# Performance work log

Hardware: AMD Instinct MI355X
Metric: run time of the kernel (lower is better)

The kernel has to match this reference:

```python
import math
import jax, jax.numpy as jnp
import numpy as np

H, DK = 16, 64            # n_heads, d_kv
NUM_BUCKETS, MAX_DIST = 32, 128


def _relative_position_buckets(S):
    # Bidirectional (encoder) T5 bucketization of relative positions.
    ctx = jnp.arange(S, dtype=jnp.int32)[:, None]      # query positions
    mem = jnp.arange(S, dtype=jnp.int32)[None, :]      # key positions
    rp = mem - ctx                                     # [S, S]
    nb = NUM_BUCKETS // 2
    rb = (rp > 0).astype(jnp.int32) * nb
    n = jnp.abs(rp)
    max_exact = nb // 2
    is_small = n < max_exact
    large = max_exact + (
        jnp.log(jnp.maximum(n, 1).astype(jnp.float32) / max_exact)
        / math.log(MAX_DIST / max_exact)
        * (nb - max_exact)
    ).astype(jnp.int32)
    large = jnp.minimum(large, nb - 1)
    return rb + jnp.where(is_small, n, large)          # [S, S] int32


def setup_inputs() -> dict:
    key = jax.random.key(0)
    ks = jax.random.split(key, 6)
    B, S, D = 4, 1024, 1024
    inner = H * DK
    std = 0.02
    return {
        "hidden_states": jax.random.normal(ks[0], (B, S, D), jnp.float32),
        "Wq": jax.random.normal(ks[1], (inner, D), jnp.float32) * std,
        "Wk": jax.random.normal(ks[2], (inner, D), jnp.float32) * std,
        "Wv": jax.random.normal(ks[3], (inner, D), jnp.float32) * std,
        "Wo": jax.random.normal(ks[4], (D, inner), jnp.float32) * std,
        "rel_bias": jax.random.normal(ks[5], (NUM_BUCKETS, H), jnp.float32) * std,
    }


def reference(hidden_states, Wq, Wk, Wv, Wo, rel_bias):
    B, S, D = hidden_states.shape

    def proj(W):  # bias-free linear + split heads -> [B, H, S, DK]
        return (hidden_states @ W.T).reshape(B, S, H, DK).transpose(0, 2, 1, 3)

    q, k, v = proj(Wq), proj(Wk), proj(Wv)
    # T5: NO 1/sqrt(d) scaling
    scores = jnp.einsum("bhqd,bhkd->bhqk", q, k)       # [B, H, S, S]
    bias = rel_bias[_relative_position_buckets(S)]     # [S, S, H]
    scores = scores + bias.transpose(2, 0, 1)[None]    # broadcast over batch
    attn = jax.nn.softmax(scores, axis=-1)
    ctx = jnp.einsum("bhqk,bhkd->bhqd", attn, v)       # [B, H, S, DK]
    ctx = ctx.transpose(0, 2, 1, 3).reshape(B, S, H * DK)
    return ctx @ Wo.T                                  # [B, S, D]
```

## Files before the change

### kernel.cpp

```cpp
#include <hip/hip_runtime.h>

typedef _Float16 half8 __attribute__((ext_vector_type(8)));
typedef _Float16 half4_t __attribute__((ext_vector_type(4)));
typedef float f32x4 __attribute__((ext_vector_type(4)));

#define GK 1024
#define MEG (1024 * 1024)
#define LOG2E 1.44269504088896f

#define GLD16(gptr, lptr) \
    __builtin_amdgcn_global_load_lds((const __attribute__((address_space(1))) void*)(gptr), \
                                     (__attribute__((address_space(3))) void*)(lptr), 16, 0, 0)

__global__ void cvt_all_kernel(const float* __restrict__ hidden,
                               const float* __restrict__ Wq,
                               const float* __restrict__ Wk,
                               const float* __restrict__ Wv,
                               const float* __restrict__ Wo,
                               _Float16* __restrict__ ws) {
    int b = blockIdx.x;
    const float* src;
    _Float16* dst;
    if (b < 4096)      { src = hidden; dst = ws; }
    else if (b < 5120) { src = Wq; dst = ws + 4 * MEG; b -= 4096; }
    else if (b < 6144) { src = Wk; dst = ws + 5 * MEG; b -= 5120; }
    else if (b < 7168) { src = Wv; dst = ws + 6 * MEG; b -= 6144; }
    else               { src = Wo; dst = ws + 7 * MEG; b -= 7168; }
    int i = (b * 256 + threadIdx.x) * 4;
    f32x4 v = *(const f32x4*)(src + i);
    half4_t h;
    h[0] = (_Float16)v[0]; h[1] = (_Float16)v[1];
    h[2] = (_Float16)v[2]; h[3] = (_Float16)v[3];
    *(half4_t*)(dst + i) = h;
}

__global__ __launch_bounds__(256) void gemm_qkv_kernel(
    const _Float16* __restrict__ A,
    const _Float16* __restrict__ B0,
    const _Float16* __restrict__ B1,
    const _Float16* __restrict__ B2,
    _Float16* __restrict__ O0,
    _Float16* __restrict__ O1,
    _Float16* __restrict__ O2)
{
    int z = blockIdx.z;
    const _Float16* Bw = (z == 0) ? B0 : ((z == 1) ? B1 : B2);
    _Float16* Oh = (z == 0) ? O0 : ((z == 1) ? O1 : O2);

    __shared__ __attribute__((aligned(16))) _Float16 sA[2][128][32];
    __shared__ __attribute__((aligned(16))) _Float16 sB[2][128][32];

    const int tid = threadIdx.x;
    const int wave = tid >> 6, lane = tid & 63;
    const int quad = lane >> 4, l16 = lane & 15;
    const int wr = wave >> 1, wc = wave & 1;
    const int M0 = blockIdx.y * 128, N0 = blockIdx.x * 128;

    const int rl = lane >> 2;
    const int cl = (lane & 3) * 8;
    const size_t aRow0 = (size_t)(M0 + wave * 16 + rl) * GK + cl;
    const size_t aRow1 = aRow0 + (size_t)64 * GK;
    const size_t bRow0 = (size_t)(N0 + wave * 16 + rl) * GK + cl;
    const size_t bRow1 = bRow0 + (size_t)64 * GK;
    _Float16* ldsA[2][2] = {{&sA[0][wave * 16][0], &sA[0][64 + wave * 16][0]},
                            {&sA[1][wave * 16][0], &sA[1][64 + wave * 16][0]}};
    _Float16* ldsB[2][2] = {{&sB[0][wave * 16][0], &sB[0][64 + wave * 16][0]},
                            {&sB[1][wave * 16][0], &sB[1][64 + wave * 16][0]}};

    f32x4 acc[4][4] = {};

    for (int kt = 0; kt < GK / 64; ++kt) {
        const int ko = kt * 64;
        #pragma unroll
        for (int c = 0; c < 2; ++c) {
            GLD16(A + aRow0 + ko + c * 32, ldsA[c][0]);
            GLD16(A + aRow1 + ko + c * 32, ldsA[c][1]);
            GLD16(Bw + bRow0 + ko + c * 32, ldsB[c][0]);
            GLD16(Bw + bRow1 + ko + c * 32, ldsB[c][1]);
        }
        __syncthreads();
        #pragma unroll
        for (int c = 0; c < 2; ++c) {
            half8 af[4], bf[4];
            #pragma unroll
            for (int i = 0; i < 4; ++i)
                af[i] = *(const half8*)&sA[c][wr * 64 + i * 16 + l16][quad * 8];
            #pragma unroll
            for (int j = 0; j < 4; ++j)
                bf[j] = *(const half8*)&sB[c][wc * 64 + j * 16 + l16][quad * 8];
            #pragma unroll
            for (int i = 0; i < 4; ++i)
                #pragma unroll
                for (int j = 0; j < 4; ++j)
                    acc[i][j] = __builtin_amdgcn_mfma_f32_16x16x32_f16(af[i], bf[j], acc[i][j], 0, 0, 0);
        }
        __syncthreads();
    }

    #pragma unroll
    for (int i = 0; i < 4; ++i) {
        #pragma unroll
        for (int j = 0; j < 4; ++j) {
            #pragma unroll
            for (int r = 0; r < 4; ++r) {
                int m = M0 + wr * 64 + i * 16 + quad * 4 + r;
                int n = N0 + wc * 64 + j * 16 + l16;
                int b = m >> 10, s = m & 1023, hh = n >> 6, d = n & 63;
                Oh[((size_t)((b * 16 + hh) * 1024 + s)) * 64 + d] = (_Float16)acc[i][j][r];
            }
        }
    }
}

__global__ __launch_bounds__(256) void gemm_o_kernel(
    const _Float16* __restrict__ A,
    const _Float16* __restrict__ Bw,
    float* __restrict__ Of)
{
    __shared__ __attribute__((aligned(16))) _Float16 sA[2][64][32];
    __shared__ __attribute__((aligned(16))) _Float16 sB[2][128][32];

    const int tid = threadIdx.x;
    const int wave = tid >> 6, lane = tid & 63;
    const int quad = lane >> 4, l16 = lane & 15;
    const int M0 = blockIdx.y * 64, N0 = blockIdx.x * 128;

    const int rl = lane >> 2;
    const int cl = (lane & 3) * 8;
    const size_t aRow  = (size_t)(M0 + wave * 16 + rl) * GK + cl;
    const size_t bRow0 = (size_t)(N0 + wave * 16 + rl) * GK + cl;
    const size_t bRow1 = bRow0 + (size_t)64 * GK;
    _Float16* ldsA[2]    = {&sA[0][wave * 16][0], &sA[1][wave * 16][0]};
    _Float16* ldsB[2][2] = {{&sB[0][wave * 16][0], &sB[0][64 + wave * 16][0]},
                            {&sB[1][wave * 16][0], &sB[1][64 + wave * 16][0]}};

    f32x4 acc[4][2] = {};

    for (int kt = 0; kt < GK / 64; ++kt) {
        const int ko = kt * 64;
        #pragma unroll
        for (int c = 0; c < 2; ++c) {
            GLD16(A + aRow + ko + c * 32, ldsA[c]);
            GLD16(Bw + bRow0 + ko + c * 32, ldsB[c][0]);
            GLD16(Bw + bRow1 + ko + c * 32, ldsB[c][1]);
        }
        __syncthreads();
        #pragma unroll
        for (int c = 0; c < 2; ++c) {
            half8 af[4], bf[2];
            #pragma unroll
            for (int i = 0; i < 4; ++i)
                af[i] = *(const half8*)&sA[c][i * 16 + l16][quad * 8];
            #pragma unroll
            for (int j = 0; j < 2; ++j)
                bf[j] = *(const half8*)&sB[c][wave * 32 + j * 16 + l16][quad * 8];
            #pragma unroll
            for (int i = 0; i < 4; ++i)
                #pragma unroll
                for (int j = 0; j < 2; ++j)
                    acc[i][j] = __builtin_amdgcn_mfma_f32_16x16x32_f16(af[i], bf[j], acc[i][j], 0, 0, 0);
        }
        __syncthreads();
    }

    #pragma unroll
    for (int i = 0; i < 4; ++i) {
        #pragma unroll
        for (int j = 0; j < 2; ++j) {
            #pragma unroll
            for (int r = 0; r < 4; ++r) {
                int m = M0 + i * 16 + quad * 4 + r;
                int n = N0 + wave * 32 + j * 16 + l16;
                Of[(size_t)m * 1024 + n] = acc[i][j][r];
            }
        }
    }
}

__global__ __launch_bounds__(256) void transpose_v_kernel(
    const _Float16* __restrict__ V, _Float16* __restrict__ VT) {
    __shared__ _Float16 tile[64][65];
    const int s0 = blockIdx.x * 64;
    const int bh = blockIdx.y;
    const _Float16* Vb = V + (size_t)bh * 1024 * 64;
    _Float16* Tb = VT + (size_t)bh * 64 * 1024;
    const int tr = threadIdx.x >> 6;
    const int tc = threadIdx.x & 63;
    #pragma unroll
    for (int i = 0; i < 16; ++i) {
        int r = i * 4 + tr;
        tile[r][tc] = Vb[(size_t)(s0 + r) * 64 + tc];
    }
    __syncthreads();
    #pragma unroll
    for (int i = 0; i < 16; ++i) {
        int d = i * 4 + tr;
        Tb[(size_t)d * 1024 + s0 + tc] = tile[tc][d];
    }
}

#define MAXTREE(mx, s) do {                                          \
    float t0_ = fmaxf(fmaxf(s[0][0], s[0][1]), s[0][2]);             \
    float t1_ = fmaxf(fmaxf(s[0][3], s[1][0]), s[1][1]);             \
    float t2_ = fmaxf(fmaxf(s[1][2], s[1][3]), s[2][0]);             \
    float t3_ = fmaxf(fmaxf(s[2][1], s[2][2]), s[2][3]);             \
    float t4_ = fmaxf(fmaxf(s[3][0], s[3][1]), s[3][2]);             \
    mx = fmaxf(fmaxf(fmaxf(t0_, t1_), fmaxf(t2_, t3_)),              \
               fmaxf(t4_, s[3][3]));                                 \
} while (0)

__device__ __forceinline__ float emit_p(const f32x4* sc, float kk,
                                        _Float16* sProw, int quad) {
    float ps0 = 0.0f, ps1 = 0.0f;
    #pragma unroll
    for (int j = 0; j < 4; ++j) {
        half4_t pw;
        float pj = 0.0f;
        #pragma unroll
        for (int r = 0; r < 4; ++r) {
            float p = __builtin_exp2f(__builtin_fmaf(sc[j][r], LOG2E, kk));
            pj += p;
            pw[r] = (_Float16)p;
        }
        if (j & 1) ps1 += pj; else ps0 += pj;
        *(half4_t*)&sProw[j * 16 + quad * 4] = pw;
    }
    return ps0 + ps1;
}

__global__ __launch_bounds__(256) void attn_kernel(
    const _Float16* __restrict__ Q,
    const _Float16* __restrict__ K,
    const _Float16* __restrict__ VT,
    const float* __restrict__ rel_bias,
    _Float16* __restrict__ ctx)
{
    const int S = 1024;
    const int wid = blockIdx.x;
    const int xcd = wid & 7;
    const int rr = wid >> 3;
    const int qt = rr & 15;
    const int g = xcd + 8 * (rr >> 4);
    const int h = g & 15;
    const int b = g >> 4;
    const int q0 = qt * 64;
    const int bh = b * 16 + h;
    const _Float16* Qh = Q + (size_t)bh * S * 64;
    const _Float16* Kh = K + (size_t)bh * S * 64;
    const _Float16* VTh = VT + (size_t)bh * 64 * S;

    __shared__ __attribute__((aligned(16))) _Float16 sK[64][72];
    __shared__ __attribute__((aligned(16))) _Float16 sVt[64][72];
    __shared__ __attribute__((aligned(16))) _Float16 sP[4][16][72];
    __shared__ _Float16 sBias[1088];

    const int tid = threadIdx.x;
    const int wave = tid >> 6, lane = tid & 63;
    const int quad = lane >> 4, l16 = lane & 15;

    for (int i = tid; i < 1087; i += 256) {
        int delta = i - (q0 + 63);
        int rb = (delta > 0) ? 16 : 0;
        int n = (delta < 0) ? -delta : delta;
        int bucket;
        if (n < 8) bucket = rb + n;
        else bucket = rb + 8 + (n >= 12) + (n >= 16) + (n >= 23) + (n >= 32)
                             + (n >= 46) + (n >= 64) + (n >= 91);
        sBias[i] = (_Float16)rel_bias[bucket * 16 + h];
    }

    half8 qf0 = *(const half8*)(Qh + (size_t)(q0 + wave * 16 + l16) * 64 + quad * 8);
    half8 qf1 = *(const half8*)(Qh + (size_t)(q0 + wave * 16 + l16) * 64 + 32 + quad * 8);

    const int sr = tid >> 3;
    const int sc_ = (tid & 7) * 8;
    const _Float16* kp0 = Kh + (size_t)sr * 64 + sc_;
    const _Float16* kp1 = kp0 + (size_t)32 * 64;
    const _Float16* vp0 = VTh + (size_t)sr * S + sc_;
    const _Float16* vp1 = vp0 + (size_t)32 * S;
    _Float16* sKw0 = &sK[sr][sc_];
    _Float16* sKw1 = &sK[sr + 32][sc_];
    _Float16* sVw0 = &sVt[sr][sc_];
    _Float16* sVw1 = &sVt[sr + 32][sc_];

    half8 rk0 = *(const half8*)kp0;
    half8 rk1 = *(const half8*)kp1;
    half8 rv0 = *(const half8*)vp0;
    half8 rv1 = *(const half8*)vp1;
    kp0 += 4096; kp1 += 4096; vp0 += 64; vp1 += 64;

    float m_run = -INFINITY, l_run = 0.0f;
    f32x4 acc[4] = {};

    for (int kt = 0; kt < 16; ++kt) {
        __syncthreads();
        *(half8*)sKw0 = rk0;
        *(half8*)sKw1 = rk1;
        *(half8*)sVw0 = rv0;
        *(half8*)sVw1 = rv1;
        __syncthreads();
        if (kt < 15) {
            rk0 = *(const half8*)kp0;
            rk1 = *(const half8*)kp1;
            rv0 = *(const half8*)vp0;
            rv1 = *(const half8*)vp1;
            kp0 += 4096; kp1 += 4096; vp0 += 64; vp1 += 64;
        }

        f32x4 sc[4] = {};
        #pragma unroll
        for (int j = 0; j < 4; ++j) {
            half8 kf0 = *(const half8*)&sK[j * 16 + l16][quad * 8];
            half8 kf1 = *(const half8*)&sK[j * 16 + l16][32 + quad * 8];
            sc[j] = __builtin_amdgcn_mfma_f32_16x16x32_f16(kf0, qf0, sc[j], 0, 0, 0);
            sc[j] = __builtin_amdgcn_mfma_f32_16x16x32_f16(kf1, qf1, sc[j], 0, 0, 0);
        }

        const int bbase = kt * 64 + quad * 4 - wave * 16 - l16 + 63;
        if (kt <= qt - 3 || kt >= qt + 3) {
            const float cb = (float)sBias[bbase];
            float mx; MAXTREE(mx, sc);
            if (__all(mx + cb <= m_run + 8.0f)) {
                l_run += emit_p(sc, (cb - m_run) * LOG2E, &sP[wave][l16][0], quad);
            } else {
                mx = fmaxf(mx, __shfl_xor(mx, 16));
                mx = fmaxf(mx, __shfl_xor(mx, 32));
                float mnew = fmaxf(m_run, mx + cb);
                float alpha = __expf(m_run - mnew);
                float ps = emit_p(sc, (cb - mnew) * LOG2E, &sP[wave][l16][0], quad);
                m_run = mnew;
                l_run = l_run * alpha + ps;
                #pragma unroll
                for (int dt = 0; dt < 4; ++dt) acc[dt] *= alpha;
            }
        } else {
            #pragma unroll
            for (int j = 0; j < 4; ++j)
                #pragma unroll
                for (int r = 0; r < 4; ++r)
                    sc[j][r] += (float)sBias[bbase + j * 16 + r];
            float mx; MAXTREE(mx, sc);
            if (__all(mx <= m_run + 8.0f)) {
                l_run += emit_p(sc, -m_run * LOG2E, &sP[wave][l16][0], quad);
            } else {
                mx = fmaxf(mx, __shfl_xor(mx, 16));
                mx = fmaxf(mx, __shfl_xor(mx, 32));
                float mnew = fmaxf(m_run, mx);
                float alpha = __expf(m_run - mnew);
                float ps = emit_p(sc, -mnew * LOG2E, &sP[wave][l16][0], quad);
                m_run = mnew;
                l_run = l_run * alpha + ps;
                #pragma unroll
                for (int dt = 0; dt < 4; ++dt) acc[dt] *= alpha;
            }
        }

        half8 pf0 = *(const half8*)&sP[wave][l16][quad * 8];
        half8 pf1 = *(const half8*)&sP[wave][l16][32 + quad * 8];
        #pragma unroll
        for (int dt = 0; dt < 4; ++dt) {
            half8 vf0 = *(const half8*)&sVt[dt * 16 + l16][quad * 8];
            half8 vf1 = *(const half8*)&sVt[dt * 16 + l16][32 + quad * 8];
            acc[dt] = __builtin_amdgcn_mfma_f32_16x16x32_f16(vf0, pf0, acc[dt], 0, 0, 0);
            acc[dt] = __builtin_amdgcn_mfma_f32_16x16x32_f16(vf1, pf1, acc[dt], 0, 0, 0);
        }
    }

    l_run += __shfl_xor(l_run, 16);
    l_run += __shfl_xor(l_run, 32);
    const float inv = 1.0f / l_run;
    const size_t qg = (size_t)(b * 1024 + q0 + wave * 16 + l16);
    #pragma unroll
    for (int dt = 0; dt < 4; ++dt) {
        half4_t o;
        #pragma unroll
        for (int r = 0; r < 4; ++r) o[r] = (_Float16)(acc[dt][r] * inv);
        *(half4_t*)&ctx[qg * 1024 + h * 64 + dt * 16 + quad * 4] = o;
    }
}

extern "C" void kernel_launch(void* const* d_in, const int* in_sizes, int n_in,
                              void* d_out, int out_size, void* d_ws, size_t ws_size,
                              hipStream_t stream) {
    const float* hidden   = (const float*)d_in[0];
    const float* Wq       = (const float*)d_in[1];
    const float* Wk       = (const float*)d_in[2];
    const float* Wv       = (const float*)d_in[3];
    const float* Wo       = (const float*)d_in[4];
    const float* rel_bias = (const float*)d_in[5];
    float* out = (float*)d_out;

    _Float16* ws    = (_Float16*)d_ws;
    _Float16* h16   = ws;
    _Float16* wq16  = ws + 4 * (size_t)MEG;
    _Float16* wk16  = ws + 5 * (size_t)MEG;
    _Float16* wv16  = ws + 6 * (size_t)MEG;
    _Float16* wo16  = ws + 7 * (size_t)MEG;
    _Float16* Qs    = ws + 8 * (size_t)MEG;
    _Float16* Ks    = ws + 12 * (size_t)MEG;
    _Float16* Vs    = ws + 16 * (size_t)MEG;
    _Float16* ctx16 = ws + 20 * (size_t)MEG;
    _Float16* VTs   = h16;

    cvt_all_kernel<<<8192, 256, 0, stream>>>(hidden, Wq, Wk, Wv, Wo, ws);

    gemm_qkv_kernel<<<dim3(8, 32, 3), 256, 0, stream>>>(
        h16, wq16, wk16, wv16, Qs, Ks, Vs);

    transpose_v_kernel<<<dim3(16, 64), 256, 0, stream>>>(Vs, VTs);

    attn_kernel<<<dim3(1024), 256, 0, stream>>>(Qs, Ks, VTs, rel_bias, ctx16);

    gemm_o_kernel<<<dim3(8, 64), 256, 0, stream>>>(ctx16, wo16, out);
}
```

Baseline: 201.0 us.

## Load K and V MFMA fragments directly from global memory, dropping LDS staging

```diff
diff --git a/kernel.cpp b/kernel.cpp
--- a/kernel.cpp
+++ b/kernel.cpp
@@ -249,8 +249,6 @@
     const _Float16* Kh = K + (size_t)bh * S * 64;
     const _Float16* VTh = VT + (size_t)bh * 64 * S;
 
-    __shared__ __attribute__((aligned(16))) _Float16 sK[64][72];
-    __shared__ __attribute__((aligned(16))) _Float16 sVt[64][72];
     __shared__ __attribute__((aligned(16))) _Float16 sP[4][16][72];
     __shared__ _Float16 sBias[1088];
 
@@ -272,48 +270,43 @@
     half8 qf0 = *(const half8*)(Qh + (size_t)(q0 + wave * 16 + l16) * 64 + quad * 8);
     half8 qf1 = *(const half8*)(Qh + (size_t)(q0 + wave * 16 + l16) * 64 + 32 + quad * 8);
 
-    const int sr = tid >> 3;
-    const int sc_ = (tid & 7) * 8;
-    const _Float16* kp0 = Kh + (size_t)sr * 64 + sc_;
-    const _Float16* kp1 = kp0 + (size_t)32 * 64;
-    const _Float16* vp0 = VTh + (size_t)sr * S + sc_;
-    const _Float16* vp1 = vp0 + (size_t)32 * S;
-    _Float16* sKw0 = &sK[sr][sc_];
-    _Float16* sKw1 = &sK[sr + 32][sc_];
-    _Float16* sVw0 = &sVt[sr][sc_];
-    _Float16* sVw1 = &sVt[sr + 32][sc_];
-
-    half8 rk0 = *(const half8*)kp0;
-    half8 rk1 = *(const half8*)kp1;
-    half8 rv0 = *(const half8*)vp0;
-    half8 rv1 = *(const half8*)vp1;
-    kp0 += 4096; kp1 += 4096; vp0 += 64; vp1 += 64;
+    const _Float16* kbase = Kh + (size_t)l16 * 64 + quad * 8;
+    const _Float16* vbase = VTh + (size_t)l16 * 1024 + quad * 8;
+
+    __syncthreads();
+
+    half8 kf[8];
+    #pragma unroll
+    for (int j = 0; j < 4; ++j) {
+        kf[j * 2]     = *(const half8*)(kbase + j * 1024);
+        kf[j * 2 + 1] = *(const half8*)(kbase + j * 1024 + 32);
+    }
 
     float m_run = -INFINITY, l_run = 0.0f;
     f32x4 acc[4] = {};
 
     for (int kt = 0; kt < 16; ++kt) {
-        __syncthreads();
-        *(half8*)sKw0 = rk0;
-        *(half8*)sKw1 = rk1;
-        *(half8*)sVw0 = rv0;
-        *(half8*)sVw1 = rv1;
-        __syncthreads();
+        half8 vf[8];
+        #pragma unroll
+        for (int dt = 0; dt < 4; ++dt) {
+            vf[dt * 2]     = *(const half8*)(vbase + dt * 16384 + kt * 64);
+            vf[dt * 2 + 1] = *(const half8*)(vbase + dt * 16384 + kt * 64 + 32);
+        }
+
+        f32x4 sc[4] = {};
+        #pragma unroll
+        for (int j = 0; j < 4; ++j) {
+            sc[j] = __builtin_amdgcn_mfma_f32_16x16x32_f16(kf[j * 2], qf0, sc[j], 0, 0, 0);
+            sc[j] = __builtin_amdgcn_mfma_f32_16x16x32_f16(kf[j * 2 + 1], qf1, sc[j], 0, 0, 0);
+        }
+
         if (kt < 15) {
-            rk0 = *(const half8*)kp0;
-            rk1 = *(const half8*)kp1;
-            rv0 = *(const half8*)vp0;
-            rv1 = *(const half8*)vp1;
-            kp0 += 4096; kp1 += 4096; vp0 += 64; vp1 += 64;
-        }
-
-        f32x4 sc[4] = {};
-        #pragma unroll
-        for (int j = 0; j < 4; ++j) {
-            half8 kf0 = *(const half8*)&sK[j * 16 + l16][quad * 8];
-            half8 kf1 = *(const half8*)&sK[j * 16 + l16][32 + quad * 8];
-            sc[j] = __builtin_amdgcn_mfma_f32_16x16x32_f16(kf0, qf0, sc[j], 0, 0, 0);
-            sc[j] = __builtin_amdgcn_mfma_f32_16x16x32_f16(kf1, qf1, sc[j], 0, 0, 0);
+            const _Float16* kn = kbase + (kt + 1) * 4096;
+            #pragma unroll
+            for (int j = 0; j < 4; ++j) {
+                kf[j * 2]     = *(const half8*)(kn + j * 1024);
+                kf[j * 2 + 1] = *(const half8*)(kn + j * 1024 + 32);
+            }
         }
 
         const int bbase = kt * 64 + quad * 4 - wave * 16 - l16 + 63;
@@ -359,10 +352,8 @@
         half8 pf1 = *(const half8*)&sP[wave][l16][32 + quad * 8];
         #pragma unroll
         for (int dt = 0; dt < 4; ++dt) {
-            half8 vf0 = *(const half8*)&sVt[dt * 16 + l16][quad * 8];
-            half8 vf1 = *(const half8*)&sVt[dt * 16 + l16][32 + quad * 8];
-            acc[dt] = __builtin_amdgcn_mfma_f32_16x16x32_f16(vf0, pf0, acc[dt], 0, 0, 0);
-            acc[dt] = __builtin_amdgcn_mfma_f32_16x16x32_f16(vf1, pf1, acc[dt], 0, 0, 0);
+            acc[dt] = __builtin_amdgcn_mfma_f32_16x16x32_f16(vf[dt * 2], pf0, acc[dt], 0, 0, 0);
+            acc[dt] = __builtin_amdgcn_mfma_f32_16x16x32_f16(vf[dt * 2 + 1], pf1, acc[dt], 0, 0, 0);
         }
     }
 
```

Measured after the change: 267.9 us. 33.3% more time.
